# Kernel tuning notes

Measured on AMD Instinct MI355X. Metric: run time of the kernel, lower is better.

Reference implementation:

```python
import jax, jax.numpy as jnp
import numpy as np

DIM = 256
HEADS = 8
HD = DIM // HEADS        # head_dim = 32
WS = 8                   # window_size (Wh = Ww = 8)
NEXP = 8                 # num_experts
HID = 128                # attr_hidden_size (router hidden)
SCALE = HD ** -0.5


def _window_partition(x, ws):
    # (B, H, W, C) -> (B * H//ws * W//ws, ws, ws, C)
    B, H, W, C = x.shape
    x = x.reshape(B, H // ws, ws, W // ws, ws, C)
    return x.transpose(0, 1, 3, 2, 4, 5).reshape(-1, ws, ws, C)


def _window_reverse(w, ws, B, H, W):
    # inverse of _window_partition
    C = w.shape[-1]
    x = w.reshape(B, H // ws, W // ws, ws, ws, C)
    return x.transpose(0, 1, 3, 2, 4, 5).reshape(B, H, W, C)


def _rope2(x):
    # 2D rotary embedding over a window: x (B*, Wh, Ww, d).
    # First d/2 channels rotated by row position, last d/2 by column position.
    B, Wh, Ww, d = x.shape
    d2 = d // 2

    def angles(L, dd):
        inv = 1.0 / (10000.0 ** (jnp.arange(0, dd, 2, dtype=jnp.float32) / dd))
        return jnp.arange(L, dtype=jnp.float32)[:, None] * inv[None, :]  # (L, dd//2)

    def rotate(v, ang, bshape):
        # v: (B, Wh, Ww, dd) pairs interleaved; ang broadcast as bshape
        p = v.reshape(*v.shape[:-1], -1, 2)
        c = jnp.cos(ang).reshape(bshape)
        s = jnp.sin(ang).reshape(bshape)
        o0 = p[..., 0] * c - p[..., 1] * s
        o1 = p[..., 0] * s + p[..., 1] * c
        return jnp.stack([o0, o1], axis=-1).reshape(v.shape)

    ah = angles(Wh, d2)  # (Wh, d2//2)
    aw = angles(Ww, d2)  # (Ww, d2//2)
    xh = rotate(x[..., :d2], ah, (1, Wh, 1, d2 // 2))
    xw = rotate(x[..., d2:], aw, (1, 1, Ww, d2 // 2))
    return jnp.concatenate([xh, xw], axis=-1)


def _moe_linear(xf, routes, w, b):
    # Top-1 dispatch: per-expert dense GEMM, masked select (jit-safe, static shapes).
    # xf: (T, in), routes: (T,) int, w: (E, out, in), b: (E, out)
    out = jnp.zeros((xf.shape[0], w.shape[1]), xf.dtype)
    for i in range(w.shape[0]):
        y = xf @ w[i].T + b[i]
        out = jnp.where((routes == i)[:, None], y, out)
    return out


def setup_inputs() -> dict:
    key = jax.random.key(0)
    ks = jax.random.split(key, 8)
    sc = 0.02
    return {
        "x": jax.random.normal(ks[0], (8, 64, 64, DIM), jnp.float32),
        "router_w1": jax.random.normal(ks[1], (HID, DIM), jnp.float32) * sc,
        "router_b1": jnp.zeros((HID,), jnp.float32),
        "router_w2": jax.random.normal(ks[2], (NEXP, HID), jnp.float32) * sc,
        "router_b2": jnp.zeros((NEXP,), jnp.float32),
        "qkv_w": jax.random.normal(ks[3], (NEXP, 3 * DIM, DIM), jnp.float32) * sc,
        "qkv_b": jnp.zeros((NEXP, 3 * DIM), jnp.float32),
        "proj_w": jax.random.normal(ks[4], (NEXP, DIM, DIM), jnp.float32) * sc,
        "proj_b": jnp.zeros((NEXP, DIM), jnp.float32),
    }


def reference(x, router_w1, router_b1, router_w2, router_b2,
              qkv_w, qkv_b, proj_w, proj_b):
    Bs, H, W, C = x.shape
    xf = x.reshape(-1, C)  # (T, C), T = Bs*H*W

    # --- Top-1 router (eval mode: no noise, no token dropping) ---
    h = jax.nn.relu(xf @ router_w1.T + router_b1)
    router_logits = h @ router_w2.T + router_b2          # (T, E)
    router_probs = jax.nn.softmax(router_logits, axis=-1)
    route_prob_max = jnp.max(router_probs, axis=-1)       # (T,)
    routes = jnp.argmax(router_probs, axis=-1)            # (T,)

    # --- per-expert QKV projection (grouped dispatch) ---
    qkv = _moe_linear(xf, routes, qkv_w, qkv_b)           # (T, 3C)
    qkv = qkv.reshape(Bs, H, W, 3 * C)

    # --- window partition (shift=0, dilated=1 -> no roll, mask=None) ---
    qw = _window_partition(qkv, WS).reshape(-1, WS * WS, 3 * C)
    B_, N, _ = qw.shape
    qkv5 = qw.reshape(B_, N, 3, HEADS, HD).transpose(2, 0, 3, 1, 4)  # (3,B_,h,N,hd)
    q, k, v = qkv5[0], qkv5[1], qkv5[2]

    # --- RoPE on q, k over the 2D window ---
    q = _rope2(q.reshape(-1, WS, WS, HD)).reshape(B_, HEADS, N, HD)
    k = _rope2(k.reshape(-1, WS, WS, HD)).reshape(B_, HEADS, N, HD)

    # --- windowed attention (moe_mask is all zeros in eval: no drops) ---
    attn = jax.nn.softmax((q * SCALE) @ k.swapaxes(-2, -1), axis=-1)  # (B_,h,N,N)
    out = (attn @ v).swapaxes(1, 2).reshape(B_, N, C)

    # --- window reverse ---
    out = _window_reverse(out.reshape(-1, WS, WS, C), WS, Bs, H, W)

    # --- per-expert output projection + Switch-style prob scaling ---
    of = _moe_linear(out.reshape(-1, C), routes, proj_w, proj_b)
    of = of * route_prob_max[:, None]
    return of.reshape(Bs, H, W, C)
```

## Files before the change

kernel.cpp:

```cpp
#include <hip/hip_runtime.h>
#include <hip/hip_bf16.h>

typedef unsigned short u16;
typedef unsigned int u32;
typedef __attribute__((ext_vector_type(8))) short short8;
typedef __attribute__((ext_vector_type(4))) float f32x4;

#define T_TOK 32768
#define SCALE_ATT 0.17677669529663687f

__device__ __forceinline__ u16 f2bf(float f){
  u32 u = __float_as_uint(f);
  u32 r = u + 0x7fffu + ((u >> 16) & 1u);
  return (u16)(r >> 16);
}
__device__ __forceinline__ float bf2f(u16 h){
  return __uint_as_float(((u32)h) << 16);
}

__device__ __forceinline__ int xcd_swz(int flat, int nwg){
  return (flat & 7) * (nwg >> 3) + (flat >> 3);
}

__device__ __forceinline__ void gl16(const u16* g, u16* l){
  __builtin_amdgcn_global_load_lds(
      (const __attribute__((address_space(1))) u32*)g,
      (__attribute__((address_space(3))) u32*)l, 16, 0, 0);
}

__global__ __launch_bounds__(256) void k_router(
    const float* __restrict__ x, const float* __restrict__ rw1,
    const float* __restrict__ b1, const float* __restrict__ w2, const float* __restrict__ b2,
    int* __restrict__ routes, float* __restrict__ pmax, int* __restrict__ counts,
    u16* __restrict__ x_bf,
    const float* __restrict__ qkvw, u16* __restrict__ qw_bf,
    const float* __restrict__ projw, u16* __restrict__ pw_bf)
{
  __shared__ __align__(16) char smem[64*132*4];
  int tid = threadIdx.x;

  if (blockIdx.x >= 512){
    int b = blockIdx.x - 512;
    if (b < 1536){
      int i = b * 256 + tid;
      float4 v = ((const float4*)qkvw)[i];
      ushort4 o;
      o.x = f2bf(v.x); o.y = f2bf(v.y); o.z = f2bf(v.z); o.w = f2bf(v.w);
      ((ushort4*)qw_bf)[i] = o;
    } else {
      int i = (b - 1536) * 256 + tid;
      float4 v = ((const float4*)projw)[i];
      ushort4 o;
      o.x = f2bf(v.x); o.y = f2bf(v.y); o.z = f2bf(v.z); o.w = f2bf(v.w);
      ((ushort4*)pw_bf)[i] = o;
    }
    return;
  }

  u16* Ah = (u16*)smem;
  u16* Al = Ah + 2560;
  u16* Bh = Al + 2560;
  u16* Bl = Bh + 5120;
  float* Hs = (float*)smem;
  __shared__ int lhist[8];

  int t0 = blockIdx.x * 64;
  int wv = tid >> 6, lane = tid & 63, quad = lane >> 4, l16 = lane & 15;
  if (tid < 8) lhist[tid] = 0;

  int arow = tid >> 2, acg = tid & 3;
  int brow = tid >> 1, bhalf = tid & 1;

  f32x4 acc[4][2];
  #pragma unroll
  for (int i = 0; i < 4; ++i)
    #pragma unroll
    for (int j = 0; j < 2; ++j)
      #pragma unroll
      for (int rr = 0; rr < 4; ++rr) acc[i][j][rr] = 0.f;

  for (int kt = 0; kt < 8; ++kt){
    const float* gx = x + (size_t)(t0 + arow) * 256 + kt * 32 + acg * 8;
    float4 v0 = *(const float4*)gx;
    float4 v1 = *(const float4*)(gx + 4);
    ushort4 h0, h1, l0, l1;
    h0.x = f2bf(v0.x); h0.y = f2bf(v0.y); h0.z = f2bf(v0.z); h0.w = f2bf(v0.w);
    h1.x = f2bf(v1.x); h1.y = f2bf(v1.y); h1.z = f2bf(v1.z); h1.w = f2bf(v1.w);
    l0.x = f2bf(v0.x - bf2f(h0.x)); l0.y = f2bf(v0.y - bf2f(h0.y));
    l0.z = f2bf(v0.z - bf2f(h0.z)); l0.w = f2bf(v0.w - bf2f(h0.w));
    l1.x = f2bf(v1.x - bf2f(h1.x)); l1.y = f2bf(v1.y - bf2f(h1.y));
    l1.z = f2bf(v1.z - bf2f(h1.z)); l1.w = f2bf(v1.w - bf2f(h1.w));
    u16* gxb = x_bf + (size_t)(t0 + arow) * 256 + kt * 32 + acg * 8;
    *(ushort4*)gxb = h0; *(ushort4*)(gxb + 4) = h1;
    const float* gw = rw1 + (size_t)brow * 256 + kt * 32 + bhalf * 16;
    ushort4 wh[4], wl[4];
    #pragma unroll
    for (int q = 0; q < 4; ++q){
      float4 wf = *(const float4*)(gw + q*4);
      wh[q].x = f2bf(wf.x); wh[q].y = f2bf(wf.y); wh[q].z = f2bf(wf.z); wh[q].w = f2bf(wf.w);
      wl[q].x = f2bf(wf.x - bf2f(wh[q].x)); wl[q].y = f2bf(wf.y - bf2f(wh[q].y));
      wl[q].z = f2bf(wf.z - bf2f(wh[q].z)); wl[q].w = f2bf(wf.w - bf2f(wh[q].w));
    }
    __syncthreads();
    *(ushort4*)&Ah[arow*40 + acg*8    ] = h0;
    *(ushort4*)&Ah[arow*40 + acg*8 + 4] = h1;
    *(ushort4*)&Al[arow*40 + acg*8    ] = l0;
    *(ushort4*)&Al[arow*40 + acg*8 + 4] = l1;
    #pragma unroll
    for (int q = 0; q < 4; ++q){
      *(ushort4*)&Bh[brow*40 + bhalf*16 + q*4] = wh[q];
      *(ushort4*)&Bl[brow*40 + bhalf*16 + q*4] = wl[q];
    }
    __syncthreads();
    short8 ah[4], al[4], bhf[2], blf[2];
    #pragma unroll
    for (int i = 0; i < 4; ++i){
      ah[i] = *(const short8*)&Ah[(i*16 + l16)*40 + quad*8];
      al[i] = *(const short8*)&Al[(i*16 + l16)*40 + quad*8];
    }
    #pragma unroll
    for (int j = 0; j < 2; ++j){
      bhf[j] = *(const short8*)&Bh[(wv*32 + j*16 + l16)*40 + quad*8];
      blf[j] = *(const short8*)&Bl[(wv*32 + j*16 + l16)*40 + quad*8];
    }
    #pragma unroll
    for (int i = 0; i < 4; ++i)
      #pragma unroll
      for (int j = 0; j < 2; ++j){
        acc[i][j] = __builtin_amdgcn_mfma_f32_16x16x32_bf16(ah[i], bhf[j], acc[i][j], 0, 0, 0);
        acc[i][j] = __builtin_amdgcn_mfma_f32_16x16x32_bf16(ah[i], blf[j], acc[i][j], 0, 0, 0);
        acc[i][j] = __builtin_amdgcn_mfma_f32_16x16x32_bf16(al[i], bhf[j], acc[i][j], 0, 0, 0);
      }
  }
  __syncthreads();

  #pragma unroll
  for (int i = 0; i < 4; ++i)
    #pragma unroll
    for (int j = 0; j < 2; ++j){
      int col = wv*32 + j*16 + l16;
      float bb = b1[col];
      #pragma unroll
      for (int rr = 0; rr < 4; ++rr){
        float h = acc[i][j][rr] + bb;
        Hs[(i*16 + quad*4 + rr)*132 + col] = h > 0.f ? h : 0.f;
      }
    }
  __syncthreads();

  #pragma unroll
  for (int pass = 0; pass < 2; ++pass){
    int mtok = (tid >> 3) + pass * 32;
    int e = tid & 7;
    const float4* w2r = (const float4*)(w2 + e * 128);
    float l = b2[e];
    #pragma unroll
    for (int k4 = 0; k4 < 32; ++k4){
      float4 w = w2r[k4];
      int k = k4 * 4;
      l = fmaf(Hs[mtok*132+k  ], w.x, l);
      l = fmaf(Hs[mtok*132+k+1], w.y, l);
      l = fmaf(Hs[mtok*132+k+2], w.z, l);
      l = fmaf(Hs[mtok*132+k+3], w.w, l);
    }
    float mv = l; int mi = e;
    #pragma unroll
    for (int off = 1; off < 8; off <<= 1){
      float ov = __shfl_xor(mv, off, 64);
      int   oi = __shfl_xor(mi, off, 64);
      if (ov > mv || (ov == mv && oi < mi)){ mv = ov; mi = oi; }
    }
    float sum = expf(l - mv);
    #pragma unroll
    for (int off = 1; off < 8; off <<= 1) sum += __shfl_xor(sum, off, 64);
    if (e == 0){
      int t = t0 + mtok;
      routes[t] = mi;
      pmax[t] = 1.0f / sum;
      atomicAdd(&lhist[mi], 1);
    }
  }
  __syncthreads();
  if (tid < 8 && lhist[tid] > 0) atomicAdd(&counts[tid], lhist[tid]);
}

__global__ __launch_bounds__(256) void k_scatter(
    const int* __restrict__ routes, const int* __restrict__ counts,
    int* __restrict__ cursors, int* __restrict__ sorted, int* __restrict__ rank,
    int* __restrict__ offs)
{
  __shared__ int lc[8], lb[8], so[9];
  int tid = threadIdx.x;
  if (tid == 0){
    int o = 0; so[0] = 0;
    #pragma unroll
    for (int e = 0; e < 8; ++e){ o += ((counts[e] + 127) >> 7) << 7; so[e+1] = o; }
  }
  if (tid < 8) lc[tid] = 0;
  __syncthreads();
  int t = blockIdx.x * 256 + tid;
  int e = routes[t];
  int rl = atomicAdd(&lc[e], 1);
  __syncthreads();
  if (tid < 8 && lc[tid] > 0) lb[tid] = atomicAdd(&cursors[tid], lc[tid]);
  __syncthreads();
  int pos = so[e] + lb[e] + rl;
  sorted[pos] = t;
  rank[t] = pos;
  if (blockIdx.x == 0 && tid < 9) offs[tid] = so[tid];
}

template<int NOUT, bool PROJ, int NB, int NWG>
__global__ __launch_bounds__(256) void k_gemm(
    const u16* __restrict__ A, const u16* __restrict__ W,
    const float* __restrict__ bias, const int* __restrict__ sidx,
    const int* __restrict__ offs, const float* __restrict__ pmax,
    u16* __restrict__ outb, float* __restrict__ outf)
{
  __shared__ __align__(1024) u16 As[2][4096];
  __shared__ __align__(1024) u16 Bs[2][4096];
  int tid = threadIdx.x;
  int flat = blockIdx.y * NB + blockIdx.x;
  int logical = xcd_swz(flat, NWG);
  int m0 = (logical / NB) * 128;
  int n0 = (logical % NB) * 128;
  int total = offs[8];
  if (m0 >= total) return;
  int e = 0;
  #pragma unroll
  for (int i = 1; i < 8; ++i) if (m0 >= offs[i]) e = i;

  int wv = tid >> 6, lane = tid & 63, quad = lane >> 4, l16 = lane & 15;
  int wrow = (wv >> 1) * 64, wcol = (wv & 1) * 64;

  int srow = wv*16 + (lane >> 2);
  int cg = (lane & 3) ^ ((srow >> 1) & 3);
  const u16 *ag0, *ag1;
  if (PROJ){
    ag0 = A + (size_t)(m0 + srow) * 256 + cg * 8;
    ag1 = A + (size_t)(m0 + srow + 64) * 256 + cg * 8;
  } else {
    int tA0 = sidx[m0 + srow];      if (tA0 < 0) tA0 = 0;
    int tA1 = sidx[m0 + srow + 64]; if (tA1 < 0) tA1 = 0;
    ag0 = A + (size_t)tA0 * 256 + cg * 8;
    ag1 = A + (size_t)tA1 * 256 + cg * 8;
  }
  int pc = (srow >> 4) + (srow & 15) * 4;
  const u16* bg0 = W + ((size_t)e * NOUT + n0 + pc) * 256 + cg * 8;
  const u16* bg1 = W + ((size_t)e * NOUT + n0 + 64 + pc) * 256 + cg * 8;

  f32x4 acc[4][4];
  #pragma unroll
  for (int i = 0; i < 4; ++i)
    #pragma unroll
    for (int j = 0; j < 4; ++j)
      #pragma unroll
      for (int r = 0; r < 4; ++r) acc[i][j][r] = 0.f;

  int qsw8 = (quad ^ ((l16 >> 1) & 3)) * 8;

  {
    u16* a_lo = (u16*)((char*)&As[0][0] + wv*1024);
    u16* b_lo = (u16*)((char*)&Bs[0][0] + wv*1024);
    gl16(ag0, a_lo);  gl16(ag1, (u16*)((char*)a_lo + 4096));
    gl16(bg0, b_lo);  gl16(bg1, (u16*)((char*)b_lo + 4096));
  }

  #pragma unroll
  for (int kt = 0; kt < 8; ++kt){
    int cur = kt & 1;
    __syncthreads();
    if (kt < 7){
      u16* a_lo = (u16*)((char*)&As[cur^1][0] + wv*1024);
      u16* b_lo = (u16*)((char*)&Bs[cur^1][0] + wv*1024);
      gl16(ag0 + (kt+1)*32, a_lo);
      gl16(ag1 + (kt+1)*32, (u16*)((char*)a_lo + 4096));
      gl16(bg0 + (kt+1)*32, b_lo);
      gl16(bg1 + (kt+1)*32, (u16*)((char*)b_lo + 4096));
    }
    short8 af[4], bfv[4];
    #pragma unroll
    for (int i = 0; i < 4; ++i)
      af[i] = *(const short8*)&As[cur][(wrow + i*16 + l16)*32 + qsw8];
    #pragma unroll
    for (int j = 0; j < 4; ++j)
      bfv[j] = *(const short8*)&Bs[cur][(wcol + j*16 + l16)*32 + qsw8];
    #pragma unroll
    for (int i = 0; i < 4; ++i)
      #pragma unroll
      for (int j = 0; j < 4; ++j)
        acc[i][j] = __builtin_amdgcn_mfma_f32_16x16x32_bf16(af[i], bfv[j], acc[i][j], 0, 0, 0);
  }

  float4 bj4 = *(const float4*)&bias[e*NOUT + n0 + wcol + l16*4];
  if (PROJ){
    #pragma unroll
    for (int i = 0; i < 4; ++i){
      #pragma unroll
      for (int ri = 0; ri < 4; ++ri){
        int row = wrow + i*16 + quad*4 + ri;
        int t = sidx[m0 + row];
        if (t < 0) continue;
        float pm = pmax[t];
        float4 ov;
        ov.x = (acc[i][0][ri] + bj4.x) * pm;
        ov.y = (acc[i][1][ri] + bj4.y) * pm;
        ov.z = (acc[i][2][ri] + bj4.z) * pm;
        ov.w = (acc[i][3][ri] + bj4.w) * pm;
        *(float4*)&outf[(size_t)t * NOUT + n0 + wcol + l16*4] = ov;
      }
    }
  } else {
    int col0 = n0 + wcol + l16*4;
    bool isqk = (col0 < 512);
    float inv0 = 0.f, inv1 = 0.f;
    float qsc = (col0 < 256) ? SCALE_ATT : 1.0f;
    if (isqk){
      int p0 = (col0 & 15) >> 1;
      inv0 = __expf(-1.1512925465f * (float)p0);
      inv1 = inv0 * 0.31622776601683794f;
    }
    int sel  = col0 >> 8;
    int head = (col0 >> 5) & 7;
    int ch   = col0 & 31;
    size_t hb = ((size_t)(sel * 8 + head) * 512) * 2048 + ch;
    #pragma unroll
    for (int i = 0; i < 4; ++i){
      #pragma unroll
      for (int ri = 0; ri < 4; ++ri){
        int row = wrow + i*16 + quad*4 + ri;
        int t = sidx[m0 + row];
        if (t < 0) continue;
        float vx = acc[i][0][ri] + bj4.x;
        float vy = acc[i][1][ri] + bj4.y;
        float vz = acc[i][2][ri] + bj4.z;
        float vw = acc[i][3][ri] + bj4.w;
        if (isqk){
          float pos = (float)((col0 & 16) ? (t & 7) : ((t >> 6) & 7));
          float a0r = pos * inv0, a1r = pos * inv1;
          float s0, c0s, s1, c1s;
          __sincosf(a0r, &s0, &c0s);
          __sincosf(a1r, &s1, &c1s);
          float r0 = (vx*c0s - vy*s0) * qsc;
          float r1 = (vx*s0 + vy*c0s) * qsc;
          float r2 = (vz*c1s - vw*s1) * qsc;
          float r3 = (vz*s1 + vw*c1s) * qsc;
          vx = r0; vy = r1; vz = r2; vw = r3;
        }
        int win = (t >> 12) * 64 + ((t >> 9) & 7) * 8 + ((t >> 3) & 7);
        int n   = ((t >> 6) & 7) * 8 + (t & 7);
        uint2 ov;
        ov.x = (u32)f2bf(vx) | ((u32)f2bf(vy) << 16);
        ov.y = (u32)f2bf(vz) | ((u32)f2bf(vw) << 16);
        *(uint2*)&outb[hb + (size_t)win * 2048 + n * 32] = ov;
      }
    }
  }
}

__global__ __launch_bounds__(64, 3) void k_attn(const u16* __restrict__ qkv,
                                                const int* __restrict__ rank,
                                                u16* __restrict__ attn_s)
{
  __shared__ __align__(16) u16 Ps[64*72];
  __shared__ __align__(16) u16 Vt[32*72];

  int lane = threadIdx.x;
  int quad = lane >> 4, l16 = lane & 15;
  int wh = xcd_swz(blockIdx.x, 4096);
  int head = wh >> 9, win = wh & 511;
  int b = win >> 6, wy = (win >> 3) & 7, wx = win & 7;
  int tb = b*4096 + wy*512 + wx*8;

  const u16* qbase = qkv + (size_t)(head * 512 + win) * 2048;
  const u16* kbase = qbase + (size_t)8 * 512 * 2048;
  const u16* vbase = qbase + (size_t)16 * 512 * 2048;

  int rk[4][4];
  #pragma unroll
  for (int i = 0; i < 4; ++i)
    #pragma unroll
    for (int rr = 0; rr < 4; ++rr){
      int m = i*16 + quad*4 + rr;
      rk[i][rr] = rank[tb + (m >> 3) * 64 + (m & 7)];
    }

  short8 qf[4], kf[4];
  #pragma unroll
  for (int i = 0; i < 4; ++i){
    qf[i] = *(const short8*)(qbase + (i*16 + l16)*32 + quad*8);
    kf[i] = *(const short8*)(kbase + (i*16 + l16)*32 + quad*8);
  }
  uint4 va[4];
  #pragma unroll
  for (int h = 0; h < 4; ++h)
    va[h] = *(const uint4*)(vbase + h*512 + l16*32 + quad*8);

  f32x4 sa[4][4];
  #pragma unroll
  for (int i = 0; i < 4; ++i)
    #pragma unroll
    for (int j = 0; j < 4; ++j){
      #pragma unroll
      for (int rr = 0; rr < 4; ++rr) sa[i][j][rr] = 0.f;
      sa[i][j] = __builtin_amdgcn_mfma_f32_16x16x32_bf16(qf[i], kf[j], sa[i][j], 0, 0, 0);
    }

  f32x4 rs[4];
  #pragma unroll
  for (int i = 0; i < 4; ++i)
    #pragma unroll
    for (int rr = 0; rr < 4; ++rr){
      float e0 = __expf(sa[i][0][rr]);
      float e1 = __expf(sa[i][1][rr]);
      float e2 = __expf(sa[i][2][rr]);
      float e3 = __expf(sa[i][3][rr]);
      rs[i][rr] = (e0 + e1) + (e2 + e3);
      uint2 pk;
      pk.x = (u32)f2bf(e0) | ((u32)f2bf(e1) << 16);
      pk.y = (u32)f2bf(e2) | ((u32)f2bf(e3) << 16);
      *(uint2*)&Ps[(i*16 + quad*4 + rr)*72 + l16*4] = pk;
    }
  #pragma unroll
  for (int i = 0; i < 4; ++i)
    #pragma unroll
    for (int rr = 0; rr < 4; ++rr){
      #pragma unroll
      for (int off = 1; off < 16; off <<= 1)
        rs[i][rr] += __shfl_xor(rs[i][rr], off, 64);
    }

  u32* vu = (u32*)va;
  #pragma unroll
  for (int h = 0; h < 4; ++h){
    int pn = l16 * 4 + h;
    #pragma unroll
    for (int w = 0; w < 4; ++w){
      u32 vv = vu[h*4 + w];
      Vt[(quad*8 + 2*w    )*72 + pn] = (u16)(vv & 0xffff);
      Vt[(quad*8 + 2*w + 1)*72 + pn] = (u16)(vv >> 16);
    }
  }

  f32x4 oa[4][2];
  #pragma unroll
  for (int i = 0; i < 4; ++i)
    #pragma unroll
    for (int rr = 0; rr < 4; ++rr){ oa[i][0][rr] = 0.f; oa[i][1][rr] = 0.f; }
  #pragma unroll
  for (int ks = 0; ks < 2; ++ks){
    short8 vf0 = *(const short8*)&Vt[(     l16)*72 + ks*32 + quad*8];
    short8 vf1 = *(const short8*)&Vt[(16 + l16)*72 + ks*32 + quad*8];
    #pragma unroll
    for (int i = 0; i < 4; ++i){
      short8 pf = *(const short8*)&Ps[(i*16 + l16)*72 + ks*32 + quad*8];
      oa[i][0] = __builtin_amdgcn_mfma_f32_16x16x32_bf16(pf, vf0, oa[i][0], 0, 0, 0);
      oa[i][1] = __builtin_amdgcn_mfma_f32_16x16x32_bf16(pf, vf1, oa[i][1], 0, 0, 0);
    }
  }

  #pragma unroll
  for (int i = 0; i < 4; ++i)
    #pragma unroll
    for (int rr = 0; rr < 4; ++rr){
      float inv = __builtin_amdgcn_rcpf(rs[i][rr]);
      int pos = rk[i][rr];
      u16* op = attn_s + (size_t)pos * 256 + head * 32 + l16;
      op[0]  = f2bf(oa[i][0][rr] * inv);
      op[16] = f2bf(oa[i][1][rr] * inv);
    }
}

extern "C" void kernel_launch(void* const* d_in, const int* in_sizes, int n_in,
                              void* d_out, int out_size, void* d_ws, size_t ws_size,
                              hipStream_t stream){
  const float* x     = (const float*)d_in[0];
  const float* rw1   = (const float*)d_in[1];
  const float* rb1   = (const float*)d_in[2];
  const float* rw2   = (const float*)d_in[3];
  const float* rb2   = (const float*)d_in[4];
  const float* qkvw  = (const float*)d_in[5];
  const float* qkvb  = (const float*)d_in[6];
  const float* projw = (const float*)d_in[7];
  const float* projb = (const float*)d_in[8];
  float* out = (float*)d_out;

  char* ws = (char*)d_ws;
  u16*   x_bf    = (u16*)(ws);
  u16*   qkv_bf  = (u16*)(ws + 16777216);
  u16*   attn_s  = (u16*)(ws + 67108864);
  u16*   qw_bf   = (u16*)(ws + 84410368);
  u16*   pw_bf   = (u16*)(ws + 87556096);
  int*   routes  = (int*)(ws + 88604672);
  float* pmaxp   = (float*)(ws + 88735744);
  int*   sorted  = (int*)(ws + 88866816);
  int*   rank    = (int*)(ws + 89001984);
  int*   counts  = (int*)(ws + 89133056);
  int*   cursors = (int*)(ws + 89133056 + 32);
  int*   offs    = (int*)(ws + 89133056 + 64);

  hipMemsetAsync(counts, 0, 64, stream);
  hipMemsetAsync(sorted, 0xFF, 135168, stream);
  k_router<<<2560, 256, 0, stream>>>(x, rw1, rb1, rw2, rb2, routes, pmaxp, counts,
                                     x_bf, qkvw, qw_bf, projw, pw_bf);
  k_scatter<<<128, 256, 0, stream>>>(routes, counts, cursors, sorted, rank, offs);
  k_gemm<768, false, 6, 1584><<<dim3(6, 264), 256, 0, stream>>>(
      x_bf, qw_bf, qkvb, sorted, offs, nullptr, qkv_bf, nullptr);
  k_attn<<<4096, 64, 0, stream>>>(qkv_bf, rank, attn_s);
  k_gemm<256, true, 2, 528><<<dim3(2, 264), 256, 0, stream>>>(
      attn_s, pw_bf, projb, sorted, offs, pmaxp, nullptr, out);
}
```

Before: 199.7 us.

## Triple-buffer MoE GEMM LDS loads and prefetch router GEMM inputs into registers

The expert GEMM moves from double to triple buffering. Global-to-LDS loads are issued two K-tiles ahead, and each step waits with an explicit vmcnt followed by a barrier, so only the tile about to be used must have landed. The router GEMM also loads the next K-slice of x and rw1 into registers before computing on the current one, hiding global load latency. The cost is more LDS per block (48KB vs 32KB), which may reduce occupancy, plus reliance on hand-written waitcnt counts being correct.

```diff
diff --git a/kernel.cpp b/kernel.cpp
--- a/kernel.cpp
+++ b/kernel.cpp
@@ -79,10 +79,18 @@
       #pragma unroll
       for (int rr = 0; rr < 4; ++rr) acc[i][j][rr] = 0.f;
 
+  const float* gx_base = x + (size_t)(t0 + arow) * 256 + acg * 8;
+  u16* gxb_base = x_bf + (size_t)(t0 + arow) * 256 + acg * 8;
+  const float* gw_base = rw1 + (size_t)brow * 256 + bhalf * 16;
+
+  float4 v0 = *(const float4*)gx_base;
+  float4 v1 = *(const float4*)(gx_base + 4);
+  float4 wf0 = *(const float4*)(gw_base     );
+  float4 wf1 = *(const float4*)(gw_base +  4);
+  float4 wf2 = *(const float4*)(gw_base +  8);
+  float4 wf3 = *(const float4*)(gw_base + 12);
+
   for (int kt = 0; kt < 8; ++kt){
-    const float* gx = x + (size_t)(t0 + arow) * 256 + kt * 32 + acg * 8;
-    float4 v0 = *(const float4*)gx;
-    float4 v1 = *(const float4*)(gx + 4);
     ushort4 h0, h1, l0, l1;
     h0.x = f2bf(v0.x); h0.y = f2bf(v0.y); h0.z = f2bf(v0.z); h0.w = f2bf(v0.w);
     h1.x = f2bf(v1.x); h1.y = f2bf(v1.y); h1.z = f2bf(v1.z); h1.w = f2bf(v1.w);
@@ -90,16 +98,27 @@
     l0.z = f2bf(v0.z - bf2f(h0.z)); l0.w = f2bf(v0.w - bf2f(h0.w));
     l1.x = f2bf(v1.x - bf2f(h1.x)); l1.y = f2bf(v1.y - bf2f(h1.y));
     l1.z = f2bf(v1.z - bf2f(h1.z)); l1.w = f2bf(v1.w - bf2f(h1.w));
-    u16* gxb = x_bf + (size_t)(t0 + arow) * 256 + kt * 32 + acg * 8;
-    *(ushort4*)gxb = h0; *(ushort4*)(gxb + 4) = h1;
-    const float* gw = rw1 + (size_t)brow * 256 + kt * 32 + bhalf * 16;
+    *(ushort4*)(gxb_base + kt*32)     = h0;
+    *(ushort4*)(gxb_base + kt*32 + 4) = h1;
     ushort4 wh[4], wl[4];
-    #pragma unroll
-    for (int q = 0; q < 4; ++q){
-      float4 wf = *(const float4*)(gw + q*4);
-      wh[q].x = f2bf(wf.x); wh[q].y = f2bf(wf.y); wh[q].z = f2bf(wf.z); wh[q].w = f2bf(wf.w);
-      wl[q].x = f2bf(wf.x - bf2f(wh[q].x)); wl[q].y = f2bf(wf.y - bf2f(wh[q].y));
-      wl[q].z = f2bf(wf.z - bf2f(wh[q].z)); wl[q].w = f2bf(wf.w - bf2f(wh[q].w));
+    {
+      float4 wf;
+      wf = wf0;
+      wh[0].x = f2bf(wf.x); wh[0].y = f2bf(wf.y); wh[0].z = f2bf(wf.z); wh[0].w = f2bf(wf.w);
+      wl[0].x = f2bf(wf.x - bf2f(wh[0].x)); wl[0].y = f2bf(wf.y - bf2f(wh[0].y));
+      wl[0].z = f2bf(wf.z - bf2f(wh[0].z)); wl[0].w = f2bf(wf.w - bf2f(wh[0].w));
+      wf = wf1;
+      wh[1].x = f2bf(wf.x); wh[1].y = f2bf(wf.y); wh[1].z = f2bf(wf.z); wh[1].w = f2bf(wf.w);
+      wl[1].x = f2bf(wf.x - bf2f(wh[1].x)); wl[1].y = f2bf(wf.y - bf2f(wh[1].y));
+      wl[1].z = f2bf(wf.z - bf2f(wh[1].z)); wl[1].w = f2bf(wf.w - bf2f(wh[1].w));
+      wf = wf2;
+      wh[2].x = f2bf(wf.x); wh[2].y = f2bf(wf.y); wh[2].z = f2bf(wf.z); wh[2].w = f2bf(wf.w);
+      wl[2].x = f2bf(wf.x - bf2f(wh[2].x)); wl[2].y = f2bf(wf.y - bf2f(wh[2].y));
+      wl[2].z = f2bf(wf.z - bf2f(wh[2].z)); wl[2].w = f2bf(wf.w - bf2f(wh[2].w));
+      wf = wf3;
+      wh[3].x = f2bf(wf.x); wh[3].y = f2bf(wf.y); wh[3].z = f2bf(wf.z); wh[3].w = f2bf(wf.w);
+      wl[3].x = f2bf(wf.x - bf2f(wh[3].x)); wl[3].y = f2bf(wf.y - bf2f(wh[3].y));
+      wl[3].z = f2bf(wf.z - bf2f(wh[3].z)); wl[3].w = f2bf(wf.w - bf2f(wh[3].w));
     }
     __syncthreads();
     *(ushort4*)&Ah[arow*40 + acg*8    ] = h0;
@@ -112,6 +131,14 @@
       *(ushort4*)&Bl[brow*40 + bhalf*16 + q*4] = wl[q];
     }
     __syncthreads();
+    if (kt < 7){
+      v0  = *(const float4*)(gx_base + (kt+1)*32);
+      v1  = *(const float4*)(gx_base + (kt+1)*32 + 4);
+      wf0 = *(const float4*)(gw_base + (kt+1)*32);
+      wf1 = *(const float4*)(gw_base + (kt+1)*32 + 4);
+      wf2 = *(const float4*)(gw_base + (kt+1)*32 + 8);
+      wf3 = *(const float4*)(gw_base + (kt+1)*32 + 12);
+    }
     short8 ah[4], al[4], bhf[2], blf[2];
     #pragma unroll
     for (int i = 0; i < 4; ++i){
@@ -217,8 +244,8 @@
     const int* __restrict__ offs, const float* __restrict__ pmax,
     u16* __restrict__ outb, float* __restrict__ outf)
 {
-  __shared__ __align__(1024) u16 As[2][4096];
-  __shared__ __align__(1024) u16 Bs[2][4096];
+  __shared__ __align__(1024) u16 As[3][4096];
+  __shared__ __align__(1024) u16 Bs[3][4096];
   int tid = threadIdx.x;
   int flat = blockIdx.y * NB + blockIdx.x;
   int logical = xcd_swz(flat, NWG);
@@ -259,25 +286,27 @@
 
   int qsw8 = (quad ^ ((l16 >> 1) & 3)) * 8;
 
-  {
-    u16* a_lo = (u16*)((char*)&As[0][0] + wv*1024);
-    u16* b_lo = (u16*)((char*)&Bs[0][0] + wv*1024);
-    gl16(ag0, a_lo);  gl16(ag1, (u16*)((char*)a_lo + 4096));
-    gl16(bg0, b_lo);  gl16(bg1, (u16*)((char*)b_lo + 4096));
-  }
+#define STAGE_KT(kt, buf) do { \
+    u16* a_lo = (u16*)((char*)&As[(buf)][0] + wv*1024); \
+    u16* b_lo = (u16*)((char*)&Bs[(buf)][0] + wv*1024); \
+    gl16(ag0 + (kt)*32, a_lo); \
+    gl16(ag1 + (kt)*32, (u16*)((char*)a_lo + 4096)); \
+    gl16(bg0 + (kt)*32, b_lo); \
+    gl16(bg1 + (kt)*32, (u16*)((char*)b_lo + 4096)); \
+  } while(0)
+
+  STAGE_KT(0, 0);
+  STAGE_KT(1, 1);
 
   #pragma unroll
   for (int kt = 0; kt < 8; ++kt){
-    int cur = kt & 1;
-    __syncthreads();
-    if (kt < 7){
-      u16* a_lo = (u16*)((char*)&As[cur^1][0] + wv*1024);
-      u16* b_lo = (u16*)((char*)&Bs[cur^1][0] + wv*1024);
-      gl16(ag0 + (kt+1)*32, a_lo);
-      gl16(ag1 + (kt+1)*32, (u16*)((char*)a_lo + 4096));
-      gl16(bg0 + (kt+1)*32, b_lo);
-      gl16(bg1 + (kt+1)*32, (u16*)((char*)b_lo + 4096));
-    }
+    const int cur = kt % 3;
+    if (kt < 7) asm volatile("s_waitcnt vmcnt(4) lgkmcnt(0)" ::: "memory");
+    else        asm volatile("s_waitcnt vmcnt(0) lgkmcnt(0)" ::: "memory");
+    __builtin_amdgcn_sched_barrier(0);
+    __builtin_amdgcn_s_barrier();
+    __builtin_amdgcn_sched_barrier(0);
+    if (kt < 6) STAGE_KT(kt+2, (kt+2)%3);
     short8 af[4], bfv[4];
     #pragma unroll
     for (int i = 0; i < 4; ++i)
@@ -291,6 +320,7 @@
       for (int j = 0; j < 4; ++j)
         acc[i][j] = __builtin_amdgcn_mfma_f32_16x16x32_bf16(af[i], bfv[j], acc[i][j], 0, 0, 0);
   }
+#undef STAGE_KT
 
   float4 bj4 = *(const float4*)&bias[e*NOUT + n0 + wcol + l16*4];
   if (PROJ){
```

Result: no change. 196.4 us (-1.7%).
